# Kernel optimization log

Measured on AMD Instinct MI355X. Metric: run time of the kernel, lower is better.

Reference implementation:

```python
import jax, jax.numpy as jnp
import numpy as np

B, S = 1, 2048
D, HD, NH, NKV, L, V, FF = 2048, 256, 8, 4, 4, 32000, 8192
WINDOW = 1024
SOFTCAP = 50.0
FINAL_CAP = 30.0
EPS = 1e-6
THETA = 10000.0
ATTN_TYPES = ("local", "global", "local", "global")
NEG = -2.3819763e38
SCALE = HD ** -0.5


def _rms(x, w):
    # RMSNorm with unit offset: x * rsqrt(mean(x^2)+eps) * (1 + w)
    n = x * jax.lax.rsqrt(jnp.mean(x * x, axis=-1, keepdims=True) + EPS)
    return n * (1.0 + w)


def _rope(x, cos, sin):
    # x: [B, S, H, HD]; rotate-half formulation (Gemma pairs i with i+HD/2)
    h = HD // 2
    x1, x2 = x[..., :h], x[..., h:]
    c = cos[None, :, None, :]
    s = sin[None, :, None, :]
    return jnp.concatenate([x1 * c - x2 * s, x1 * s + x2 * c], axis=-1)


def setup_inputs() -> dict:
    key = jax.random.key(0)
    ks = jax.random.split(key, 15)
    sd = 0.02
    f = lambda k, shape: jax.random.normal(k, shape, jnp.float32) * sd
    return {
        "input_ids": jax.random.randint(ks[0], (B, S), 0, V),
        "embed": f(ks[1], (V, D)),
        "wq": f(ks[2], (L, NH * HD, D)),
        "wk": f(ks[3], (L, NKV * HD, D)),
        "wv": f(ks[4], (L, NKV * HD, D)),
        "wo": f(ks[5], (L, D, NH * HD)),
        "wg": f(ks[6], (L, FF, D)),
        "wu": f(ks[7], (L, FF, D)),
        "wd": f(ks[8], (L, D, FF)),
        "ln_in": f(ks[9], (L, D)),
        "ln_pa": f(ks[10], (L, D)),
        "ln_pf": f(ks[11], (L, D)),
        "ln_pff": f(ks[12], (L, D)),
        "ln_f": f(ks[13], (D,)),
        "w_lm": f(ks[14], (V, D)),
    }


def _forward(input_ids, embed, wq, wk, wv, wo, wg, wu, wd,
             ln_in, ln_pa, ln_pf, ln_pff, ln_f, w_lm):
    # rotary tables
    pos = jnp.arange(S, dtype=jnp.float32)
    inv = 1.0 / (THETA ** (jnp.arange(0, HD, 2, dtype=jnp.float32) / HD))
    ang = pos[:, None] * inv[None, :]
    cos, sin = jnp.cos(ang), jnp.sin(ang)  # [S, HD/2]

    # additive masks
    i = jnp.arange(S)[:, None]
    j = jnp.arange(S)[None, :]
    causal = jnp.where(j > i, NEG, 0.0).astype(jnp.float32)
    local = jnp.where((j > i) | (i - j >= WINDOW), NEG, 0.0).astype(jnp.float32)

    h = embed[input_ids] * jnp.asarray(D ** 0.5, jnp.float32)
    rep = NH // NKV
    for l in range(L):
        mask = local if ATTN_TYPES[l] == "local" else causal
        x = _rms(h, ln_in[l])
        q = jnp.einsum('bsd,od->bso', x, wq[l]).reshape(B, S, NH, HD)
        k = jnp.einsum('bsd,od->bso', x, wk[l]).reshape(B, S, NKV, HD)
        v = jnp.einsum('bsd,od->bso', x, wv[l]).reshape(B, S, NKV, HD)
        q = _rope(q, cos, sin)
        k = _rope(k, cos, sin)
        k = jnp.repeat(k, rep, axis=2)  # GQA expand
        v = jnp.repeat(v, rep, axis=2)
        q = q.transpose(0, 2, 1, 3)  # bhsd
        k = k.transpose(0, 2, 1, 3)
        v = v.transpose(0, 2, 1, 3)
        qk = jnp.einsum('bhsd,bhfd->bhsf', q, k) * SCALE
        qk = jnp.tanh(qk / SOFTCAP) * SOFTCAP  # attn logit softcap
        scores = jax.nn.softmax(qk + mask, axis=-1)
        a = jnp.einsum('bhsf,bhfd->bhsd', scores, v)
        a = a.transpose(0, 2, 1, 3).reshape(B, S, NH * HD)
        attn_out = jnp.einsum('bso,do->bsd', a, wo[l])
        h = h + _rms(attn_out, ln_pa[l])  # post-attn norm then residual
        x = _rms(h, ln_pf[l])
        gate = jax.nn.gelu(jnp.einsum('bsd,fd->bsf', x, wg[l]), approximate=True)
        up = jnp.einsum('bsd,fd->bsf', x, wu[l])
        mlp = jnp.einsum('bsf,df->bsd', gate * up, wd[l])
        h = h + _rms(mlp, ln_pff[l])
    h = _rms(h, ln_f)
    logits = jnp.einsum('bsd,vd->bsv', h, w_lm)
    return jnp.tanh(logits / FINAL_CAP) * FINAL_CAP


def reference(input_ids, embed, wq, wk, wv, wo, wg, wu, wd,
              ln_in, ln_pa, ln_pf, ln_pff, ln_f, w_lm):
    return _forward(input_ids, embed, wq, wk, wv, wo, wg, wu, wd,
                    ln_in, ln_pa, ln_pf, ln_pff, ln_f, w_lm)
```

## Files before the change

kernel.cpp:

```cpp
#include <hip/hip_runtime.h>
#include <hip/hip_bf16.h>

typedef __attribute__((ext_vector_type(8))) __bf16 bf16x8;
typedef __attribute__((ext_vector_type(4))) float floatx4;

typedef __attribute__((address_space(1))) const unsigned char kGlb;
typedef __attribute__((address_space(3))) unsigned char kLds;

static constexpr int S = 2048;
static constexpr int D = 2048;
static constexpr int HD = 256;
static constexpr int NH = 8;
static constexpr int NKV = 4;
static constexpr int NLAYER = 4;
static constexpr int VOCAB = 32000;
static constexpr int FF = 8192;
static constexpr int WINDOW = 1024;

__device__ __forceinline__ float blk_sum(float v) {
    __shared__ float sm[4];
    #pragma unroll
    for (int o = 32; o > 0; o >>= 1) v += __shfl_down(v, o, 64);
    int lane = threadIdx.x & 63, w = threadIdx.x >> 6;
    __syncthreads();
    if (lane == 0) sm[w] = v;
    __syncthreads();
    return sm[0] + sm[1] + sm[2] + sm[3];
}

__device__ __forceinline__ float blk_max(float v) {
    __shared__ float sm[4];
    #pragma unroll
    for (int o = 32; o > 0; o >>= 1) v = fmaxf(v, __shfl_down(v, o, 64));
    int lane = threadIdx.x & 63, w = threadIdx.x >> 6;
    __syncthreads();
    if (lane == 0) sm[w] = v;
    __syncthreads();
    return fmaxf(fmaxf(sm[0], sm[1]), fmaxf(sm[2], sm[3]));
}

__global__ void embed_kernel(const int* __restrict__ ids, const float* __restrict__ E,
                             float* __restrict__ h) {
    int d = blockIdx.x * 256 + threadIdx.x;
    int s = blockIdx.y;
    h[(long)s * D + d] = E[(long)ids[s] * D + d] * 45.25483399593904f;
}

__global__ void rope_table_kernel(float* __restrict__ c, float* __restrict__ sn) {
    int i = threadIdx.x;
    int p = blockIdx.x;
    float inv = powf(10000.f, -(float)i / 128.f);
    float a = (float)p * inv;
    c[p * 128 + i] = cosf(a);
    sn[p * 128 + i] = sinf(a);
}

__global__ void cvt_bf16_kernel(const float* __restrict__ src, __hip_bfloat16* __restrict__ dst,
                                long n8) {
    long stride = (long)gridDim.x * 256;
    for (long i = (long)blockIdx.x * 256 + threadIdx.x; i < n8; i += stride) {
        long o = i * 8;
        float4 a = *(const float4*)(src + o);
        float4 b = *(const float4*)(src + o + 4);
        __hip_bfloat16 h8[8] = {
            __float2bfloat16(a.x), __float2bfloat16(a.y),
            __float2bfloat16(a.z), __float2bfloat16(a.w),
            __float2bfloat16(b.x), __float2bfloat16(b.y),
            __float2bfloat16(b.z), __float2bfloat16(b.w)};
        *(uint4*)(dst + o) = *(const uint4*)h8;
    }
}

__global__ void cvt_inter_kernel(const float* __restrict__ src, __hip_bfloat16* __restrict__ dst,
                                 int half, long n8) {
    long stride = (long)gridDim.x * 256;
    for (long i = (long)blockIdx.x * 256 + threadIdx.x; i < n8; i += stride) {
        long o = i * 8;
        long row = o >> 11, col = o & 2047;
        float4 a = *(const float4*)(src + o);
        float4 b = *(const float4*)(src + o + 4);
        __hip_bfloat16 h8[8] = {
            __float2bfloat16(a.x), __float2bfloat16(a.y),
            __float2bfloat16(a.z), __float2bfloat16(a.w),
            __float2bfloat16(b.x), __float2bfloat16(b.y),
            __float2bfloat16(b.z), __float2bfloat16(b.w)};
        *(uint4*)(dst + ((row * 2 + half) << 11) + col) = *(const uint4*)h8;
    }
}

__global__ void rms_bf16_kernel(const float* __restrict__ h, const float* __restrict__ w,
                                __hip_bfloat16* __restrict__ o) {
    int s = blockIdx.x;
    const float* row = h + (long)s * D;
    float vals[8], ss = 0.f;
    #pragma unroll
    for (int t = 0; t < 8; ++t) {
        int j = t * 256 + threadIdx.x;
        float v = row[j]; vals[t] = v; ss += v * v;
    }
    ss = blk_sum(ss);
    float r = rsqrtf(ss * (1.f / D) + 1e-6f);
    #pragma unroll
    for (int t = 0; t < 8; ++t) {
        int j = t * 256 + threadIdx.x;
        o[(long)s * D + j] = __float2bfloat16(vals[t] * r * (1.f + w[j]));
    }
}

__global__ void resid_rms_kernel(float* __restrict__ h, const float* __restrict__ tt,
                                 const float* __restrict__ w) {
    int s = blockIdx.x;
    const float* row = tt + (long)s * D;
    float* hr = h + (long)s * D;
    float vals[8], ss = 0.f;
    #pragma unroll
    for (int t = 0; t < 8; ++t) {
        int j = t * 256 + threadIdx.x;
        float v = row[j]; vals[t] = v; ss += v * v;
    }
    ss = blk_sum(ss);
    float r = rsqrtf(ss * (1.f / D) + 1e-6f);
    #pragma unroll
    for (int t = 0; t < 8; ++t) {
        int j = t * 256 + threadIdx.x;
        hr[j] += vals[t] * r * (1.f + w[j]);
    }
}

__global__ void rope_kernel(__hip_bfloat16* __restrict__ x, const float* __restrict__ cb,
                            const float* __restrict__ sb, int ldx) {
    int s = blockIdx.x, hh = blockIdx.y, i = threadIdx.x;
    __hip_bfloat16* p = x + (long)s * ldx + hh * HD;
    float x1 = __bfloat162float(p[i]);
    float x2 = __bfloat162float(p[128 + i]);
    float c = cb[s * 128 + i], sn = sb[s * 128 + i];
    p[i]       = __float2bfloat16(x1 * c - x2 * sn);
    p[128 + i] = __float2bfloat16(x1 * sn + x2 * c);
}

__global__ void transpose_v_kernel(const __hip_bfloat16* __restrict__ v,
                                   __hip_bfloat16* __restrict__ vt, int ldv) {
    __shared__ ushort tile[64][65];
    int s0 = blockIdx.x * 64, d0 = blockIdx.y * 64, kv = blockIdx.z;
    const ushort* vin = (const ushort*)v;
    ushort* vout = (ushort*)vt;
    #pragma unroll
    for (int it = 0; it < 4; ++it) {
        int slot = it * 256 + threadIdx.x;
        int r = slot >> 4, c4 = (slot & 15) << 2;
        ushort4 x = *(const ushort4*)(vin + (long)(s0 + r) * ldv + kv * HD + d0 + c4);
        tile[r][c4] = x.x; tile[r][c4 + 1] = x.y; tile[r][c4 + 2] = x.z; tile[r][c4 + 3] = x.w;
    }
    __syncthreads();
    #pragma unroll
    for (int it = 0; it < 4; ++it) {
        int slot = it * 256 + threadIdx.x;
        int rr = slot >> 4, c4 = (slot & 15) << 2;
        ushort4 y;
        y.x = tile[c4][rr]; y.y = tile[c4 + 1][rr]; y.z = tile[c4 + 2][rr]; y.w = tile[c4 + 3][rr];
        *(ushort4*)(vout + (long)kv * HD * S + (long)(d0 + rr) * S + s0 + c4) = y;
    }
}

__global__ void softmax_kernel(const __hip_bfloat16* __restrict__ sc,
                               __hip_bfloat16* __restrict__ pr, int isLocal) {
    int i = blockIdx.x, hh = blockIdx.y;
    const __hip_bfloat16* row = sc + ((long)hh * S + i) * S;
    __hip_bfloat16* orow = pr + ((long)hh * S + i) * S;
    int lo = isLocal ? max(0, i - (WINDOW - 1)) : 0;
    float vals[8];
    float m = -3.0e38f;
    #pragma unroll
    for (int t = 0; t < 8; ++t) {
        int j = t * 256 + threadIdx.x;
        bool chunkAny = (t * 256 <= i) && (t * 256 + 255 >= lo);
        if (chunkAny) {
            bool valid = (j <= i) && (j >= lo);
            float v = tanhf(__bfloat162float(row[j]) * (0.0625f / 50.f)) * 50.f;
            vals[t] = valid ? v : -3.0e38f;
            m = fmaxf(m, vals[t]);
        } else {
            vals[t] = -3.0e38f;
        }
    }
    m = blk_max(m);
    float ps[8], ssum = 0.f;
    #pragma unroll
    for (int t = 0; t < 8; ++t) {
        float p = (vals[t] > -1.0e38f) ? __expf(vals[t] - m) : 0.f;
        ps[t] = p; ssum += p;
    }
    ssum = blk_sum(ssum);
    float inv = 1.f / ssum;
    #pragma unroll
    for (int t = 0; t < 8; ++t) {
        int j = t * 256 + threadIdx.x;
        orow[j] = __float2bfloat16(ps[t] * inv);
    }
}

__global__ void mul_gu_kernel(__hip_bfloat16* __restrict__ gu) {
    long idx = ((long)blockIdx.x * 256 + threadIdx.x) * 8;
    long s = idx >> 13;
    long f = idx & 8191;
    __hip_bfloat16* gp = gu + s * 16384 + f;
    const __hip_bfloat16* up = gu + s * 16384 + 8192 + f;
    uint4 gv = *(const uint4*)gp;
    uint4 uv = *(const uint4*)up;
    const __hip_bfloat16* gb = (const __hip_bfloat16*)&gv;
    const __hip_bfloat16* ub = (const __hip_bfloat16*)&uv;
    __hip_bfloat16 o[8];
    #pragma unroll
    for (int j = 0; j < 8; ++j)
        o[j] = __float2bfloat16(__bfloat162float(gb[j]) * __bfloat162float(ub[j]));
    *(uint4*)gp = *(const uint4*)o;
}

#define RD_AF(BUF, HALF)                                                          \
    {                                                                             \
        const char* _p = (const char*)&ldsA[BUF][HALF][0];                        \
        _Pragma("unroll")                                                         \
        for (int mi = 0; mi < 4; ++mi) {                                          \
            int r = wm * 64 + mi * 16 + fr;                                       \
            _Pragma("unroll")                                                     \
            for (int ks = 0; ks < 2; ++ks) {                                      \
                int c = ks * 4 + g;                                               \
                af[mi][ks] = *(const bf16x8*)(_p + r * 128 + ((c ^ (r & 7)) << 4)); \
            }                                                                     \
        }                                                                         \
    }

#define RD_BF(DST, BUF, HALF)                                                     \
    {                                                                             \
        const char* _p = (const char*)&ldsB[BUF][HALF][0];                        \
        _Pragma("unroll")                                                         \
        for (int ni = 0; ni < 2; ++ni) {                                          \
            int r = wn * 32 + ni * 16 + fr;                                       \
            _Pragma("unroll")                                                     \
            for (int ks = 0; ks < 2; ++ks) {                                      \
                int c = ks * 4 + g;                                               \
                DST[ni][ks] = *(const bf16x8*)(_p + r * 128 + ((c ^ (r & 7)) << 4)); \
            }                                                                     \
        }                                                                         \
    }

#define MM(QM, QN, BF)                                                            \
    __builtin_amdgcn_s_setprio(1);                                                \
    _Pragma("unroll")                                                             \
    for (int mi = 0; mi < 4; ++mi)                                                \
        _Pragma("unroll")                                                         \
        for (int ni = 0; ni < 2; ++ni)                                            \
            _Pragma("unroll")                                                     \
            for (int ks = 0; ks < 2; ++ks)                                        \
                acc[QM][QN][mi][ni] = __builtin_amdgcn_mfma_f32_16x16x32_bf16(    \
                    af[mi][ks], BF[ni][ks], acc[QM][QN][mi][ni], 0, 0, 0);        \
    __builtin_amdgcn_s_setprio(0);

#define PH_TAIL                                                                   \
    __builtin_amdgcn_s_barrier();                                                 \
    asm volatile("s_waitcnt lgkmcnt(0)" ::: "memory");                            \
    __builtin_amdgcn_sched_barrier(0);

#define PH_END                                                                    \
    __builtin_amdgcn_sched_barrier(0);                                            \
    __builtin_amdgcn_s_barrier();

template<int EPI>
__global__ __launch_bounds__(512, 2) void gemm_8ph(
    const __hip_bfloat16* __restrict__ A, const __hip_bfloat16* __restrict__ B,
    void* __restrict__ Cv, int K, int lda, int ldb, int ldc, int gx) {
    __shared__ __hip_bfloat16 ldsA[2][2][8192];
    __shared__ __hip_bfloat16 ldsB[2][2][8192];
    const int tid = threadIdx.x;
    const int nwg = gridDim.x;
    const int orig = blockIdx.x;
    const int wgid = (orig & 7) * (nwg >> 3) + (orig >> 3);
    const int bx = wgid % gx, by = wgid / gx;

    const __hip_bfloat16* Ab = A + (long)bx * 256 * lda;
    const __hip_bfloat16* Bb = B + (long)by * 256 * ldb;

    const int w = tid >> 6, l = tid & 63;
    const int wm = w >> 2, wn = w & 3;
    const int fr = l & 15, g = l >> 4;
    const int sRow0 = tid >> 3;
    const int sCh = tid & 7;

    floatx4 acc[2][2][4][2] = {};
    bf16x8 af[4][2], bf0[2][2], bf1[2][2];

    auto stage = [&](const __hip_bfloat16* src, int ld, int k0, __hip_bfloat16* dst) {
        #pragma unroll
        for (int i = 0; i < 2; ++i) {
            int row = sRow0 + i * 64;
            int cs = (sCh ^ (row & 7)) * 8;
            __builtin_amdgcn_global_load_lds(
                (kGlb*)(src + (long)row * ld + k0 + cs),
                (kLds*)((char*)dst + i * 8192 + tid * 16), 16, 0, 0);
        }
    };

    const int nt = K >> 6;
    const int niter = nt >> 1;

    stage(Ab,             lda, 0,  &ldsA[0][0][0]);
    stage(Bb,             ldb, 0,  &ldsB[0][0][0]);
    stage(Ab + 128 * lda, lda, 0,  &ldsA[0][1][0]);
    stage(Bb + 128 * ldb, ldb, 0,  &ldsB[0][1][0]);
    stage(Ab,             lda, 64, &ldsA[1][0][0]);
    stage(Bb,             ldb, 64, &ldsB[1][0][0]);
    asm volatile("s_waitcnt vmcnt(4)" ::: "memory");
    __builtin_amdgcn_s_barrier();

    for (int it = 0; it < niter; ++it) {
        const int t = it * 2;
        const bool last = (it == niter - 1);
        const int kN1 = (t + 1) * 64;
        const int kN2 = (t + 2) * 64;
        const int kN3 = (t + 3) * 64;
        RD_AF(0, 0);
        RD_BF(bf0, 0, 0);
        stage(Ab + 128 * lda, lda, kN1, &ldsA[1][1][0]);
        PH_TAIL
        MM(0, 0, bf0)
        PH_END
        RD_BF(bf1, 0, 1);
        stage(Bb + 128 * ldb, ldb, kN1, &ldsB[1][1][0]);
        PH_TAIL
        MM(0, 1, bf1)
        PH_END
        RD_AF(0, 1);
        if (!last) stage(Ab, lda, kN2, &ldsA[0][0][0]);
        PH_TAIL
        MM(1, 0, bf0)
        PH_END
        if (!last) stage(Bb, ldb, kN2, &ldsB[0][0][0]);
        MM(1, 1, bf1)
        __builtin_amdgcn_sched_barrier(0);
        if (last) { asm volatile("s_waitcnt vmcnt(0)" ::: "memory"); }
        else      { asm volatile("s_waitcnt vmcnt(4)" ::: "memory"); }
        __builtin_amdgcn_s_barrier();
        RD_AF(1, 0);
        RD_BF(bf0, 1, 0);
        if (!last) stage(Ab + 128 * lda, lda, kN2, &ldsA[0][1][0]);
        PH_TAIL
        MM(0, 0, bf0)
        PH_END
        RD_BF(bf1, 1, 1);
        if (!last) stage(Bb + 128 * ldb, ldb, kN2, &ldsB[0][1][0]);
        PH_TAIL
        MM(0, 1, bf1)
        PH_END
        RD_AF(1, 1);
        if (!last) stage(Ab, lda, kN3, &ldsA[1][0][0]);
        PH_TAIL
        MM(1, 0, bf0)
        PH_END
        if (!last) stage(Bb, ldb, kN3, &ldsB[1][0][0]);
        MM(1, 1, bf1)
        __builtin_amdgcn_sched_barrier(0);
        if (!last) { asm volatile("s_waitcnt vmcnt(4)" ::: "memory"); }
        __builtin_amdgcn_s_barrier();
    }

    const long cBase = (long)bx * 256 * ldc + (long)by * 256;
    const int rg = (l >> 4) * 4;
    #pragma unroll
    for (int qm = 0; qm < 2; ++qm)
    #pragma unroll
    for (int qn = 0; qn < 2; ++qn)
    #pragma unroll
    for (int mi = 0; mi < 4; ++mi)
    #pragma unroll
    for (int ni = 0; ni < 2; ++ni)
    #pragma unroll
    for (int r = 0; r < 4; ++r) {
        int row = qm * 128 + wm * 64 + mi * 16 + rg + r;
        int col = qn * 128 + wn * 32 + ni * 16 + fr;
        float v = acc[qm][qn][mi][ni][r];
        if constexpr (EPI == 3) {
            ((float*)Cv)[cBase + (long)row * ldc + col] = tanhf(v * (1.f / 30.f)) * 30.f;
        } else {
            float pv = __shfl_xor(v, 1);
            if (!(fr & 1)) {
                float gg = 0.5f * v * (1.f + tanhf(0.7978845608f * (v + 0.044715f * v * v * v)));
                long idx5 = ((long)bx * 256 + row) * (long)ldc + (long)by * 128 + (col >> 1);
                ((__hip_bfloat16*)Cv)[idx5] = __float2bfloat16(gg * pv);
            }
        }
    }
}

template<int EPI, int WM, int WN, int MI, int NI>
__global__ __launch_bounds__(WM*WN*64, 2) void gemm_pipe(
    const __hip_bfloat16* __restrict__ A, const __hip_bfloat16* __restrict__ B,
    void* __restrict__ Cv, int K, int lda, int ldb, int ldc,
    long aBatch, long bBatch, long cBatch, int bzDiv, int gx, int kMode) {
    constexpr int T  = WM * WN * 64;
    constexpr int BM = WM * MI * 16;
    constexpr int BN = WN * NI * 16;
    constexpr int AE = BM * 32;
    constexpr int BE = BN * 32;
    __shared__ __hip_bfloat16 lds[4][AE + BE];

    const int tid = threadIdx.x;
    const int nwg = gridDim.x;
    const int orig = blockIdx.x;
    const int wgid = (orig & 7) * (nwg >> 3) + (orig >> 3);
    const int bx = wgid % gx, by = wgid / gx;
    const int bz = blockIdx.z;

    int kstart = 0, kend = K;
    if (kMode == 1) { if (by > bx) return; }
    else if (kMode == 2) { if (by > bx || bx - by >= 9) return; }
    else if (kMode == 3) { kend = min(K, (bx + 1) * BM); }
    else if (kMode == 4) { kend = min(K, (bx + 1) * BM); kstart = max(0, (bx - 1024 / BM) * BM); }

    const __hip_bfloat16* Ab = A + (long)bz * aBatch + (long)bx * BM * lda;
    const __hip_bfloat16* Bb = B + (long)(bz / bzDiv) * bBatch + (long)by * BN * ldb;

    const int w = tid >> 6, l = tid & 63;
    const int wm = w / WN, wn = w % WN;
    const int wrow = wm * MI * 16, wcol = wn * NI * 16;
    const int fr = l & 15, g = l >> 4;
    const int sR = tid >> 2;
    const int sc = tid & 3;

    floatx4 acc[MI][NI] = {};
    bf16x8 bfv[NI];
    bf16x8 af[MI / 2];

    auto stageA = [&](int t, int buf) {
        const int k0 = kstart + t * 32;
        #pragma unroll
        for (int i = 0; i < 2; ++i) {
            int row = sR + i * (T / 4);
            int scol = ((sc ^ ((row >> 1) & 3)) << 3);
            __builtin_amdgcn_global_load_lds(
                (kGlb*)(Ab + (long)row * lda + k0 + scol),
                (kLds*)(&lds[buf][0] + tid * 8 + i * (T * 8)), 16, 0, 0);
        }
    };
    auto stageB = [&](int t, int buf) {
        const int k0 = kstart + t * 32;
        #pragma unroll
        for (int i = 0; i < 2; ++i) {
            int row = sR + i * (T / 4);
            int scol = ((sc ^ ((row >> 1) & 3)) << 3);
            __builtin_amdgcn_global_load_lds(
                (kGlb*)(Bb + (long)row * ldb + k0 + scol),
                (kLds*)(&lds[buf][AE] + tid * 8 + i * (T * 8)), 16, 0, 0);
        }
    };

    auto phase0 = [&](int buf, int t3, bool doStage) {
        const char* AsB = (const char*)&lds[buf][0];
        const char* BsB = (const char*)&lds[buf][AE];
        #pragma unroll
        for (int mi = 0; mi < MI / 2; ++mi) {
            int ra = wrow + mi * 16 + fr;
            af[mi] = *(const bf16x8*)(AsB + ra * 64 + ((g ^ ((ra >> 1) & 3)) << 4));
        }
        #pragma unroll
        for (int ni = 0; ni < NI; ++ni) {
            int rb = wcol + ni * 16 + fr;
            bfv[ni] = *(const bf16x8*)(BsB + rb * 64 + ((g ^ ((rb >> 1) & 3)) << 4));
        }
        if (doStage) stageA(t3, t3 & 3);
        __builtin_amdgcn_s_barrier();
        asm volatile("s_waitcnt lgkmcnt(0)" ::: "memory");
        __builtin_amdgcn_sched_barrier(0);
        __builtin_amdgcn_s_setprio(1);
        #pragma unroll
        for (int mi = 0; mi < MI / 2; ++mi)
            #pragma unroll
            for (int ni = 0; ni < NI; ++ni)
                acc[mi][ni] = __builtin_amdgcn_mfma_f32_16x16x32_bf16(af[mi], bfv[ni], acc[mi][ni], 0, 0, 0);
        __builtin_amdgcn_s_setprio(0);
        __builtin_amdgcn_sched_barrier(0);
        __builtin_amdgcn_s_barrier();
    };

    auto phase1 = [&](int buf, int t3, bool doStage, int vm) {
        const char* AsB = (const char*)&lds[buf][0];
        #pragma unroll
        for (int mi = 0; mi < MI / 2; ++mi) {
            int ra = wrow + (MI / 2 + mi) * 16 + fr;
            af[mi] = *(const bf16x8*)(AsB + ra * 64 + ((g ^ ((ra >> 1) & 3)) << 4));
        }
        if (doStage) stageB(t3, t3 & 3);
        if (vm == 8)      asm volatile("s_waitcnt vmcnt(8)" ::: "memory");
        else if (vm == 4) asm volatile("s_waitcnt vmcnt(4)" ::: "memory");
        else if (vm == 0) asm volatile("s_waitcnt vmcnt(0)" ::: "memory");
        __builtin_amdgcn_s_barrier();
        asm volatile("s_waitcnt lgkmcnt(0)" ::: "memory");
        __builtin_amdgcn_sched_barrier(0);
        __builtin_amdgcn_s_setprio(1);
        #pragma unroll
        for (int mi = 0; mi < MI / 2; ++mi)
            #pragma unroll
            for (int ni = 0; ni < NI; ++ni)
                acc[MI / 2 + mi][ni] = __builtin_amdgcn_mfma_f32_16x16x32_bf16(af[mi], bfv[ni], acc[MI / 2 + mi][ni], 0, 0, 0);
        __builtin_amdgcn_s_setprio(0);
        __builtin_amdgcn_sched_barrier(0);
        __builtin_amdgcn_s_barrier();
    };

    const int nt = (kend - kstart) >> 5;
    stageA(0, 0); stageB(0, 0);
    stageA(1, 1); stageB(1, 1);
    stageA(2, 2); stageB(2, 2);
    asm volatile("s_waitcnt vmcnt(8)" ::: "memory");
    __builtin_amdgcn_s_barrier();

    for (int t = 0; t < nt - 3; ++t) {
        const int b = t & 3;
        phase0(b, t + 3, true);
        phase1(b, t + 3, true, 8);
    }
    phase0((nt - 3) & 3, 0, false); phase1((nt - 3) & 3, 0, false, 4);
    phase0((nt - 2) & 3, 0, false); phase1((nt - 2) & 3, 0, false, 0);
    phase0((nt - 1) & 3, 0, false); phase1((nt - 1) & 3, 0, false, -1);

    const long cBase = (long)bz * cBatch + (long)bx * BM * ldc + (long)by * BN;
    const int rg = (l >> 4) * 4;
    #pragma unroll
    for (int mi = 0; mi < MI; ++mi) {
        #pragma unroll
        for (int ni = 0; ni < NI; ++ni) {
            #pragma unroll
            for (int r = 0; r < 4; ++r) {
                int row = wrow + mi * 16 + rg + r;
                int col = wcol + ni * 16 + fr;
                long idx = cBase + (long)row * ldc + col;
                float v = acc[mi][ni][r];
                if constexpr (EPI == 0) {
                    ((float*)Cv)[idx] = v;
                } else {
                    ((__hip_bfloat16*)Cv)[idx] = __float2bfloat16(v);
                }
            }
        }
    }
}

template<int EPI>
__global__ __launch_bounds__(256) void gemm_f32w(
    const __hip_bfloat16* __restrict__ A, const float* __restrict__ Bv,
    void* __restrict__ Cv, int K, int lda, int ldb, int ldc) {
    __shared__ __hip_bfloat16 As[128][32];
    __shared__ __hip_bfloat16 Bs[128][32];
    const int tid = threadIdx.x;
    const __hip_bfloat16* Ab = A + (long)blockIdx.x * 128 * lda;
    const float* Bb = Bv + (long)blockIdx.y * 128 * ldb;
    const int wid = tid >> 6, lane = tid & 63;
    const int wr = (wid >> 1) * 64, wc = (wid & 1) * 64;
    const int fr = lane & 15;
    const int kb = (lane >> 4) * 8;
    floatx4 acc[4][4] = {};
    for (int k0 = 0; k0 < K; k0 += 32) {
        __syncthreads();
        #pragma unroll
        for (int it = 0; it < 2; ++it) {
            int slot = tid + it * 256;
            int r = slot >> 2, c8 = (slot & 3) * 8;
            *reinterpret_cast<uint4*>(&As[r][c8]) =
                *reinterpret_cast<const uint4*>(Ab + (long)r * lda + k0 + c8);
        }
        #pragma unroll
        for (int it = 0; it < 4; ++it) {
            int slot = tid + it * 256;
            int r = slot >> 3, c4 = (slot & 7) * 4;
            float4 f = *reinterpret_cast<const float4*>(Bb + (long)r * ldb + k0 + c4);
            __hip_bfloat16 t4[4] = {__float2bfloat16(f.x), __float2bfloat16(f.y),
                                    __float2bfloat16(f.z), __float2bfloat16(f.w)};
            *reinterpret_cast<ushort4*>(&Bs[r][c4]) = *reinterpret_cast<const ushort4*>(t4);
        }
        __syncthreads();
        bf16x8 af[4], bfr[4];
        #pragma unroll
        for (int i = 0; i < 4; ++i)
            af[i] = *reinterpret_cast<const bf16x8*>(&As[wr + i * 16 + fr][kb]);
        #pragma unroll
        for (int j = 0; j < 4; ++j)
            bfr[j] = *reinterpret_cast<const bf16x8*>(&Bs[wc + j * 16 + fr][kb]);
        #pragma unroll
        for (int i = 0; i < 4; ++i)
            #pragma unroll
            for (int j = 0; j < 4; ++j)
                acc[i][j] = __builtin_amdgcn_mfma_f32_16x16x32_bf16(af[i], bfr[j], acc[i][j], 0, 0, 0);
    }
    const long cTile = (long)blockIdx.x * 128 * ldc + (long)blockIdx.y * 128;
    const int rg = (lane >> 4) * 4;
    #pragma unroll
    for (int i = 0; i < 4; ++i)
        #pragma unroll
        for (int j = 0; j < 4; ++j)
            #pragma unroll
            for (int r = 0; r < 4; ++r) {
                int row = wr + i * 16 + rg + r;
                int col = wc + j * 16 + fr;
                long idx = cTile + (long)row * ldc + col;
                float v = acc[i][j][r];
                if constexpr (EPI == 0) ((float*)Cv)[idx] = v;
                else if constexpr (EPI == 1) ((__hip_bfloat16*)Cv)[idx] = __float2bfloat16(v);
                else if constexpr (EPI == 2) {
                    float gg = 0.5f * v * (1.f + tanhf(0.7978845608f * (v + 0.044715f * v * v * v)));
                    ((__hip_bfloat16*)Cv)[idx] = __float2bfloat16(gg);
                } else ((float*)Cv)[idx] = tanhf(v * (1.f / 30.f)) * 30.f;
            }
}

extern "C" void kernel_launch(void* const* d_in, const int* in_sizes, int n_in,
                              void* d_out, int out_size, void* d_ws, size_t ws_size,
                              hipStream_t stream) {
    const int*   ids    = (const int*)d_in[0];
    const float* embedW = (const float*)d_in[1];
    const float* wq     = (const float*)d_in[2];
    const float* wk     = (const float*)d_in[3];
    const float* wv     = (const float*)d_in[4];
    const float* wo     = (const float*)d_in[5];
    const float* wg     = (const float*)d_in[6];
    const float* wu     = (const float*)d_in[7];
    const float* wd     = (const float*)d_in[8];
    const float* ln_in  = (const float*)d_in[9];
    const float* ln_pa  = (const float*)d_in[10];
    const float* ln_pf  = (const float*)d_in[11];
    const float* ln_pff = (const float*)d_in[12];
    const float* ln_f   = (const float*)d_in[13];
    const float* w_lm   = (const float*)d_in[14];
    float* out = (float*)d_out;

    char* ws = (char*)d_ws;
    size_t off = 0;
    auto alloc = [&](size_t bytes) -> void* {
        size_t o = (off + 255) & ~(size_t)255;
        off = o + bytes;
        return (void*)(ws + o);
    };

    float* h            = (float*)alloc((size_t)S * D * 4);
    __hip_bfloat16* xb  = (__hip_bfloat16*)alloc((size_t)S * D * 2);
    __hip_bfloat16* qkvb = (__hip_bfloat16*)alloc((size_t)S * 4096 * 2);
    __hip_bfloat16* vT  = (__hip_bfloat16*)alloc((size_t)NKV * HD * S * 2);
    __hip_bfloat16* ab  = (__hip_bfloat16*)alloc((size_t)S * NH * HD * 2);
    float* tmpf         = (float*)alloc((size_t)S * D * 4);
    __hip_bfloat16* guP = (__hip_bfloat16*)alloc((size_t)S * FF * 2);
    __hip_bfloat16* gu  = (__hip_bfloat16*)alloc((size_t)S * 16384 * 2);
    float* cosb         = (float*)alloc((size_t)S * 128 * 4);
    float* sinb         = (float*)alloc((size_t)S * 128 * 4);
    __hip_bfloat16* scores = (__hip_bfloat16*)alloc((size_t)NH * S * S * 2);
    __hip_bfloat16* probs  = (__hip_bfloat16*)alloc((size_t)NH * S * S * 2);

    const long SLq = 2048L * 2048, SLkv = 1024L * 2048, SLff = 8192L * 2048;
    const long nWlm = (long)VOCAB * D;
    __hip_bfloat16* wqkvb = (__hip_bfloat16*)alloc(4L * 4096 * 2048 * 2);
    __hip_bfloat16* wgub  = (__hip_bfloat16*)alloc(4L * 16384 * 2048 * 2);
    __hip_bfloat16* wob   = (__hip_bfloat16*)alloc(4L * SLq * 2);
    __hip_bfloat16* wdb   = (__hip_bfloat16*)alloc(4L * SLff * 2);
    __hip_bfloat16* wlmb  = (__hip_bfloat16*)alloc(nWlm * 2);
    const bool big = (off <= ws_size);
    (void)in_sizes; (void)n_in; (void)out_size;

    rope_table_kernel<<<dim3(S), dim3(128), 0, stream>>>(cosb, sinb);
    embed_kernel<<<dim3(D / 256, S), dim3(256), 0, stream>>>(ids, embedW, h);

    auto cvt = [&](const float* s, __hip_bfloat16* dp, long n) {
        long n8 = n / 8;
        long want = (n8 + 255) / 256;
        int blocks = (int)(want < 2048 ? want : 2048);
        cvt_bf16_kernel<<<dim3(blocks), dim3(256), 0, stream>>>(s, dp, n8);
    };
    auto cvtI = [&](const float* s, __hip_bfloat16* dp, int half, long n) {
        long n8 = n / 8;
        long want = (n8 + 255) / 256;
        int blocks = (int)(want < 2048 ? want : 2048);
        cvt_inter_kernel<<<dim3(blocks), dim3(256), 0, stream>>>(s, dp, half, n8);
    };
    if (big) {
        for (int l = 0; l < NLAYER; ++l) {
            cvt(wq + l * SLq,  wqkvb + (size_t)l * 4096 * 2048,                SLq);
            cvt(wk + l * SLkv, wqkvb + (size_t)l * 4096 * 2048 + 2048L * 2048, SLkv);
            cvt(wv + l * SLkv, wqkvb + (size_t)l * 4096 * 2048 + 3072L * 2048, SLkv);
            cvtI(wg + l * SLff, wgub + (size_t)l * 16384 * 2048, 0, SLff);
            cvtI(wu + l * SLff, wgub + (size_t)l * 16384 * 2048, 1, SLff);
        }
        cvt(wo, wob, 4L * SLq);
        cvt(wd, wdb, 4L * SLff);
        cvt(w_lm, wlmb, nWlm);
    }

    auto p256 = [&](int epi, const __hip_bfloat16* A, const __hip_bfloat16* B, void* C,
                    int K, int lda, int ldb, int ldc, int gx, int gy) {
        dim3 grid(gx * gy, 1, 1);
        if (epi == 3)
            gemm_8ph<3><<<grid, 512, 0, stream>>>(A, B, C, K, lda, ldb, ldc, gx);
        else
            gemm_8ph<5><<<grid, 512, 0, stream>>>(A, B, C, K, lda, ldb, ldc, gx);
    };
    auto p128 = [&](int epi, const __hip_bfloat16* A, const __hip_bfloat16* B, void* C,
                    int K, int lda, int ldb, int ldc, int gx, int gy, int gz,
                    long aB, long bB, long cB, int bzDiv, int kMode) {
        dim3 grid(gx * gy, 1, gz);
        switch (epi) {
        case 0: gemm_pipe<0, 2, 2, 4, 4><<<grid, 256, 0, stream>>>(A, B, C, K, lda, ldb, ldc, aB, bB, cB, bzDiv, gx, kMode); break;
        default: gemm_pipe<1, 2, 2, 4, 4><<<grid, 256, 0, stream>>>(A, B, C, K, lda, ldb, ldc, aB, bB, cB, bzDiv, gx, kMode); break;
        }
    };

    for (int l = 0; l < NLAYER; ++l) {
        int isLocal = (l % 2 == 0) ? 1 : 0;
        rms_bf16_kernel<<<dim3(S), dim3(256), 0, stream>>>(h, ln_in + l * D, xb);
        if (big) {
            p128(1, xb, wqkvb + (size_t)l * 4096 * 2048, qkvb, D, D, D, 4096, 16, 32, 1, 0, 0, 0, 1, 0);
        } else {
            gemm_f32w<1><<<dim3(16, 16), 256, 0, stream>>>(xb, wq + l * SLq, qkvb, D, D, D, 4096);
            gemm_f32w<1><<<dim3(16, 8), 256, 0, stream>>>(xb, wk + l * SLkv, qkvb + 2048, D, D, D, 4096);
            gemm_f32w<1><<<dim3(16, 8), 256, 0, stream>>>(xb, wv + l * SLkv, qkvb + 3072, D, D, D, 4096);
        }
        rope_kernel<<<dim3(S, NH), dim3(128), 0, stream>>>(qkvb, cosb, sinb, 4096);
        rope_kernel<<<dim3(S, NKV), dim3(128), 0, stream>>>(qkvb + 2048, cosb, sinb, 4096);
        transpose_v_kernel<<<dim3(S / 64, HD / 64, NKV), 256, 0, stream>>>(qkvb + 3072, vT, 4096);
        p128(1, qkvb, qkvb + 2048, scores, HD, 4096, 4096, S, 16, 16, NH,
             (long)HD, (long)HD, (long)S * S, 2, isLocal ? 2 : 1);
        softmax_kernel<<<dim3(S, NH), dim3(256), 0, stream>>>(scores, probs, isLocal);
        p128(1, probs, vT, ab, S, S, S, NH * HD, 16, 2, NH,
             (long)S * S, (long)HD * S, (long)HD, 2, isLocal ? 4 : 3);
        if (big) {
            p128(0, ab, wob + (size_t)l * SLq, tmpf, NH * HD, NH * HD, NH * HD, D, 16, 16, 1, 0, 0, 0, 1, 0);
        } else {
            gemm_f32w<0><<<dim3(16, 16), 256, 0, stream>>>(ab, wo + l * SLq, tmpf, NH * HD, NH * HD, NH * HD, D);
        }
        resid_rms_kernel<<<dim3(S), dim3(256), 0, stream>>>(h, tmpf, ln_pa + l * D);
        rms_bf16_kernel<<<dim3(S), dim3(256), 0, stream>>>(h, ln_pf + l * D, xb);
        if (big) {
            p256(5, xb, wgub + (size_t)l * 16384 * 2048, guP, D, D, D, FF, 8, 64);
        } else {
            gemm_f32w<2><<<dim3(16, 64), 256, 0, stream>>>(xb, wg + l * SLff, gu, D, D, D, 16384);
            gemm_f32w<1><<<dim3(16, 64), 256, 0, stream>>>(xb, wu + l * SLff, gu + 8192, D, D, D, 16384);
            mul_gu_kernel<<<dim3((S * FF) / (256 * 8)), 256, 0, stream>>>(gu);
        }
        if (big) {
            p128(0, guP, wdb + (size_t)l * SLff, tmpf, FF, FF, FF, D, 16, 16, 1, 0, 0, 0, 1, 0);
        } else {
            gemm_f32w<0><<<dim3(16, 16), 256, 0, stream>>>(gu, wd + l * SLff, tmpf, FF, 16384, FF, D);
        }
        resid_rms_kernel<<<dim3(S), dim3(256), 0, stream>>>(h, tmpf, ln_pff + l * D);
    }

    rms_bf16_kernel<<<dim3(S), dim3(256), 0, stream>>>(h, ln_f, xb);
    if (big) {
        p256(3, xb, wlmb, out, D, D, D, VOCAB, 8, VOCAB / 256);
    } else {
        gemm_f32w<3><<<dim3(16, VOCAB / 128), 256, 0, stream>>>(xb, w_lm, out, D, D, D, VOCAB);
    }
}
```

Baseline: 2.573 ms.

## Restructure 256-tile GEMM pipeline and interleave weight conversion with layers

The 8-phase GEMM main loop moves from a two-tile unrolled schedule with a triple-staged prefetch to a single-tile-per-iteration double buffer. A second A-fragment register set lets LDS reads for the next quadrant overlap the MFMA work, and finer lgkmcnt waits replace the blanket waits. The weight fp32-to-bf16 conversions now run just before each GEMM that uses them instead of all upfront, which may let conversion traffic interleave with other work and improve cache locality. The new schedule depends on hand-counted vmcnt/lgkmcnt values, so it risks subtle races or stalls if those counts are off.

```diff
diff --git a/kernel.cpp b/kernel.cpp
--- a/kernel.cpp
+++ b/kernel.cpp
@@ -216,7 +216,7 @@
     *(uint4*)gp = *(const uint4*)o;
 }
 
-#define RD_AF(BUF, HALF)                                                          \
+#define RD_AF(DST, BUF, HALF)                                                     \
     {                                                                             \
         const char* _p = (const char*)&ldsA[BUF][HALF][0];                        \
         _Pragma("unroll")                                                         \
@@ -225,7 +225,7 @@
             _Pragma("unroll")                                                     \
             for (int ks = 0; ks < 2; ++ks) {                                      \
                 int c = ks * 4 + g;                                               \
-                af[mi][ks] = *(const bf16x8*)(_p + r * 128 + ((c ^ (r & 7)) << 4)); \
+                DST[mi][ks] = *(const bf16x8*)(_p + r * 128 + ((c ^ (r & 7)) << 4)); \
             }                                                                     \
         }                                                                         \
     }
@@ -244,7 +244,7 @@
         }                                                                         \
     }
 
-#define MM(QM, QN, BF)                                                            \
+#define MM(QM, QN, AF, BF)                                                        \
     __builtin_amdgcn_s_setprio(1);                                                \
     _Pragma("unroll")                                                             \
     for (int mi = 0; mi < 4; ++mi)                                                \
@@ -253,17 +253,8 @@
             _Pragma("unroll")                                                     \
             for (int ks = 0; ks < 2; ++ks)                                        \
                 acc[QM][QN][mi][ni] = __builtin_amdgcn_mfma_f32_16x16x32_bf16(    \
-                    af[mi][ks], BF[ni][ks], acc[QM][QN][mi][ni], 0, 0, 0);        \
+                    AF[mi][ks], BF[ni][ks], acc[QM][QN][mi][ni], 0, 0, 0);        \
     __builtin_amdgcn_s_setprio(0);
-
-#define PH_TAIL                                                                   \
-    __builtin_amdgcn_s_barrier();                                                 \
-    asm volatile("s_waitcnt lgkmcnt(0)" ::: "memory");                            \
-    __builtin_amdgcn_sched_barrier(0);
-
-#define PH_END                                                                    \
-    __builtin_amdgcn_sched_barrier(0);                                            \
-    __builtin_amdgcn_s_barrier();
 
 template<int EPI>
 __global__ __launch_bounds__(512, 2) void gemm_8ph(
@@ -287,7 +278,7 @@
     const int sCh = tid & 7;
 
     floatx4 acc[2][2][4][2] = {};
-    bf16x8 af[4][2], bf0[2][2], bf1[2][2];
+    bf16x8 af[4][2], af2[4][2], bf0[2][2], bf1[2][2];
 
     auto stage = [&](const __hip_bfloat16* src, int ld, int k0, __hip_bfloat16* dst) {
         #pragma unroll
@@ -301,66 +292,64 @@
     };
 
     const int nt = K >> 6;
-    const int niter = nt >> 1;
-
-    stage(Ab,             lda, 0,  &ldsA[0][0][0]);
-    stage(Bb,             ldb, 0,  &ldsB[0][0][0]);
-    stage(Ab + 128 * lda, lda, 0,  &ldsA[0][1][0]);
-    stage(Bb + 128 * ldb, ldb, 0,  &ldsB[0][1][0]);
-    stage(Ab,             lda, 64, &ldsA[1][0][0]);
-    stage(Bb,             ldb, 64, &ldsB[1][0][0]);
+    stage(Ab,             lda, 0, &ldsA[0][0][0]);
+    stage(Bb,             ldb, 0, &ldsB[0][0][0]);
+    stage(Bb + 128 * ldb, ldb, 0, &ldsB[0][1][0]);
+    stage(Ab + 128 * lda, lda, 0, &ldsA[0][1][0]);
     asm volatile("s_waitcnt vmcnt(4)" ::: "memory");
     __builtin_amdgcn_s_barrier();
-
-    for (int it = 0; it < niter; ++it) {
-        const int t = it * 2;
-        const bool last = (it == niter - 1);
-        const int kN1 = (t + 1) * 64;
-        const int kN2 = (t + 2) * 64;
-        const int kN3 = (t + 3) * 64;
-        RD_AF(0, 0);
-        RD_BF(bf0, 0, 0);
-        stage(Ab + 128 * lda, lda, kN1, &ldsA[1][1][0]);
-        PH_TAIL
-        MM(0, 0, bf0)
-        PH_END
-        RD_BF(bf1, 0, 1);
-        stage(Bb + 128 * ldb, ldb, kN1, &ldsB[1][1][0]);
-        PH_TAIL
-        MM(0, 1, bf1)
-        PH_END
-        RD_AF(0, 1);
-        if (!last) stage(Ab, lda, kN2, &ldsA[0][0][0]);
-        PH_TAIL
-        MM(1, 0, bf0)
-        PH_END
-        if (!last) stage(Bb, ldb, kN2, &ldsB[0][0][0]);
-        MM(1, 1, bf1)
-        __builtin_amdgcn_sched_barrier(0);
-        if (last) { asm volatile("s_waitcnt vmcnt(0)" ::: "memory"); }
-        else      { asm volatile("s_waitcnt vmcnt(4)" ::: "memory"); }
+    RD_AF(af, 0, 0);
+    RD_BF(bf0, 0, 0);
+
+    for (int t = 0; t < nt; ++t) {
+        const int b = t & 1, nb = b ^ 1;
+        const int kn = (t + 1) * 64;
+        const bool last = (t == nt - 1);
+        if (!last) {
+            stage(Ab, lda, kn, &ldsA[nb][0][0]);
+            asm volatile("s_waitcnt vmcnt(4)" ::: "memory");
+        } else {
+            asm volatile("s_waitcnt vmcnt(2)" ::: "memory");
+        }
         __builtin_amdgcn_s_barrier();
-        RD_AF(1, 0);
-        RD_BF(bf0, 1, 0);
-        if (!last) stage(Ab + 128 * lda, lda, kN2, &ldsA[0][1][0]);
-        PH_TAIL
-        MM(0, 0, bf0)
-        PH_END
-        RD_BF(bf1, 1, 1);
-        if (!last) stage(Bb + 128 * ldb, ldb, kN2, &ldsB[0][1][0]);
-        PH_TAIL
-        MM(0, 1, bf1)
-        PH_END
-        RD_AF(1, 1);
-        if (!last) stage(Ab, lda, kN3, &ldsA[1][0][0]);
-        PH_TAIL
-        MM(1, 0, bf0)
-        PH_END
-        if (!last) stage(Bb, ldb, kN3, &ldsB[1][0][0]);
-        MM(1, 1, bf1)
-        __builtin_amdgcn_sched_barrier(0);
-        if (!last) { asm volatile("s_waitcnt vmcnt(4)" ::: "memory"); }
+        RD_BF(bf1, b, 1);
+        asm volatile("s_waitcnt lgkmcnt(4)" ::: "memory");
+        __builtin_amdgcn_sched_barrier(0);
+        MM(0, 0, af, bf0)
+        __builtin_amdgcn_sched_barrier(0);
+        if (!last) {
+            stage(Bb, ldb, kn, &ldsB[nb][0][0]);
+            asm volatile("s_waitcnt vmcnt(4)" ::: "memory");
+        } else {
+            asm volatile("s_waitcnt vmcnt(0)" ::: "memory");
+        }
         __builtin_amdgcn_s_barrier();
+        RD_AF(af2, b, 1);
+        asm volatile("s_waitcnt lgkmcnt(8)" ::: "memory");
+        __builtin_amdgcn_sched_barrier(0);
+        MM(0, 1, af, bf1)
+        __builtin_amdgcn_sched_barrier(0);
+        if (!last) {
+            stage(Bb + 128 * ldb, ldb, kn, &ldsB[nb][1][0]);
+            asm volatile("s_waitcnt vmcnt(4)" ::: "memory");
+        }
+        __builtin_amdgcn_s_barrier();
+        asm volatile("s_waitcnt lgkmcnt(0)" ::: "memory");
+        __builtin_amdgcn_sched_barrier(0);
+        MM(1, 0, af2, bf0)
+        __builtin_amdgcn_sched_barrier(0);
+        if (!last) {
+            stage(Ab + 128 * lda, lda, kn, &ldsA[nb][1][0]);
+            asm volatile("s_waitcnt vmcnt(4)" ::: "memory");
+        }
+        __builtin_amdgcn_s_barrier();
+        if (!last) {
+            RD_AF(af, nb, 0);
+            RD_BF(bf0, nb, 0);
+        }
+        __builtin_amdgcn_sched_barrier(0);
+        MM(1, 1, af2, bf1)
+        __builtin_amdgcn_sched_barrier(0);
     }
 
     const long cBase = (long)bx * 256 * ldc + (long)by * 256;
@@ -677,18 +666,6 @@
         int blocks = (int)(want < 2048 ? want : 2048);
         cvt_inter_kernel<<<dim3(blocks), dim3(256), 0, stream>>>(s, dp, half, n8);
     };
-    if (big) {
-        for (int l = 0; l < NLAYER; ++l) {
-            cvt(wq + l * SLq,  wqkvb + (size_t)l * 4096 * 2048,                SLq);
-            cvt(wk + l * SLkv, wqkvb + (size_t)l * 4096 * 2048 + 2048L * 2048, SLkv);
-            cvt(wv + l * SLkv, wqkvb + (size_t)l * 4096 * 2048 + 3072L * 2048, SLkv);
-            cvtI(wg + l * SLff, wgub + (size_t)l * 16384 * 2048, 0, SLff);
-            cvtI(wu + l * SLff, wgub + (size_t)l * 16384 * 2048, 1, SLff);
-        }
-        cvt(wo, wob, 4L * SLq);
-        cvt(wd, wdb, 4L * SLff);
-        cvt(w_lm, wlmb, nWlm);
-    }
 
     auto p256 = [&](int epi, const __hip_bfloat16* A, const __hip_bfloat16* B, void* C,
                     int K, int lda, int ldb, int ldc, int gx, int gy) {
@@ -712,6 +689,9 @@
         int isLocal = (l % 2 == 0) ? 1 : 0;
         rms_bf16_kernel<<<dim3(S), dim3(256), 0, stream>>>(h, ln_in + l * D, xb);
         if (big) {
+            cvt(wq + l * SLq,  wqkvb + (size_t)l * 4096 * 2048,                SLq);
+            cvt(wk + l * SLkv, wqkvb + (size_t)l * 4096 * 2048 + 2048L * 2048, SLkv);
+            cvt(wv + l * SLkv, wqkvb + (size_t)l * 4096 * 2048 + 3072L * 2048, SLkv);
             p128(1, xb, wqkvb + (size_t)l * 4096 * 2048, qkvb, D, D, D, 4096, 16, 32, 1, 0, 0, 0, 1, 0);
         } else {
             gemm_f32w<1><<<dim3(16, 16), 256, 0, stream>>>(xb, wq + l * SLq, qkvb, D, D, D, 4096);
@@ -727,6 +707,7 @@
         p128(1, probs, vT, ab, S, S, S, NH * HD, 16, 2, NH,
              (long)S * S, (long)HD * S, (long)HD, 2, isLocal ? 4 : 3);
         if (big) {
+            cvt(wo + l * SLq, wob + (size_t)l * SLq, SLq);
             p128(0, ab, wob + (size_t)l * SLq, tmpf, NH * HD, NH * HD, NH * HD, D, 16, 16, 1, 0, 0, 0, 1, 0);
         } else {
             gemm_f32w<0><<<dim3(16, 16), 256, 0, stream>>>(ab, wo + l * SLq, tmpf, NH * HD, NH * HD, NH * HD, D);
@@ -734,6 +715,8 @@
         resid_rms_kernel<<<dim3(S), dim3(256), 0, stream>>>(h, tmpf, ln_pa + l * D);
         rms_bf16_kernel<<<dim3(S), dim3(256), 0, stream>>>(h, ln_pf + l * D, xb);
         if (big) {
+            cvtI(wg + l * SLff, wgub + (size_t)l * 16384 * 2048, 0, SLff);
+            cvtI(wu + l * SLff, wgub + (size_t)l * 16384 * 2048, 1, SLff);
             p256(5, xb, wgub + (size_t)l * 16384 * 2048, guP, D, D, D, FF, 8, 64);
         } else {
             gemm_f32w<2><<<dim3(16, 64), 256, 0, stream>>>(xb, wg + l * SLff, gu, D, D, D, 16384);
@@ -741,6 +724,7 @@
             mul_gu_kernel<<<dim3((S * FF) / (256 * 8)), 256, 0, stream>>>(gu);
         }
         if (big) {
+            cvt(wd + l * SLff, wdb + (size_t)l * SLff, SLff);
             p128(0, guP, wdb + (size_t)l * SLff, tmpf, FF, FF, FF, D, 16, 16, 1, 0, 0, 0, 1, 0);
         } else {
             gemm_f32w<0><<<dim3(16, 16), 256, 0, stream>>>(gu, wd + l * SLff, tmpf, FF, 16384, FF, D);
@@ -750,6 +734,7 @@
 
     rms_bf16_kernel<<<dim3(S), dim3(256), 0, stream>>>(h, ln_f, xb);
     if (big) {
+        cvt(w_lm, wlmb, nWlm);
         p256(3, xb, wlmb, out, D, D, D, VOCAB, 8, VOCAB / 256);
     } else {
         gemm_f32w<3><<<dim3(16, VOCAB / 128), 256, 0, stream>>>(xb, w_lm, out, D, D, D, VOCAB);
```

Result: no change. 2.556 ms (-0.7%).
